# Optimization experiments

Measured on AMD Instinct MI355X. Metric: run time of the kernel, lower is better.

The kernel has to match this reference:

```python
import jax, jax.numpy as jnp
import numpy as np
import math

# dims
B, L, D = 2, 2048, 1024          # batch, seq len, embedding_dim
HID, ATT, H = 1024, 512, 8       # linear_hidden_dim, attention_dim, num_heads
DQK, DUV = ATT // H, HID // H    # 64, 128
NBUCK = 64                       # time_num_buckets
MAX_SPAN = 86400 * 90            # max_time_span
EPS = 1e-6
OUT_DIM = 2 * HID + 2 * ATT      # uvqk output dim = 3072


def _time_boundaries():
    # RelativeAttentionBiasModule._build_boundaries: pure log buckets
    steps = NBUCK - 1
    log_part = np.exp(np.linspace(0.0, math.log(MAX_SPAN), steps))
    b = np.unique(np.floor(np.clip(log_part, 1, None)).astype(np.int64)).astype(np.float32)
    return jnp.asarray(b)

_BOUNDARIES = _time_boundaries()  # len <= 63, indices < NBUCK


def setup_inputs() -> dict:
    key = jax.random.key(0)
    ks = jax.random.split(key, 8)
    x = jax.random.normal(ks[0], (B, L, D), dtype=jnp.float32)
    timestamps = jnp.sort(
        jax.random.randint(ks[1], (B, L), 0, 2592000), axis=-1
    )  # chronological event times (seconds)
    attn_mask = jnp.tril(jnp.ones((L, L), dtype=bool))[None].repeat(B, axis=0)  # causal
    W_uvqk = jax.random.normal(ks[2], (OUT_DIM, D), dtype=jnp.float32) * 0.02
    b_uvqk = jnp.zeros((OUT_DIM,), dtype=jnp.float32)
    time_bias = jax.random.normal(ks[3], (NBUCK, H), dtype=jnp.float32) * 0.02
    W_o = jax.random.normal(ks[4], (D, HID), dtype=jnp.float32) * 0.02
    b_o = jnp.zeros((D,), dtype=jnp.float32)
    rms_w = jnp.ones((HID,), dtype=jnp.float32)
    return {"x": x, "timestamps": timestamps, "attn_mask": attn_mask,
            "W_uvqk": W_uvqk, "b_uvqk": b_uvqk, "time_bias": time_bias,
            "W_o": W_o, "b_o": b_o, "rms_w": rms_w}


def reference(x, timestamps, attn_mask, W_uvqk, b_uvqk, time_bias, W_o, b_o, rms_w):
    Bx, Lx, _ = x.shape
    scale = 1.0 / math.sqrt(DQK)

    # fused uvqk projection + act1 (silu)
    h = jax.nn.silu(x @ W_uvqk.T + b_uvqk)  # [B, L, OUT_DIM]
    u, v, q, k = jnp.split(h, [HID, 2 * HID, 2 * HID + ATT], axis=-1)

    def heads(t, d):  # [B, L, H*d] -> [B, H, L, d]
        return t.reshape(Bx, Lx, H, d).transpose(0, 2, 1, 3)

    u = heads(u, DUV)
    v = heads(v, DUV)
    q = heads(q, DQK) * scale
    k = heads(k, DQK)

    logits = jnp.einsum('bhid,bhjd->bhij', q.astype(jnp.float32), k.astype(jnp.float32))

    # bucketized relative-time bias (per-head)
    tdiff = jnp.abs(timestamps[:, :, None] - timestamps[:, None, :])
    tdiff = jnp.clip(tdiff, 1, None).astype(jnp.float32)  # clamp_min(1)
    bk = jnp.searchsorted(_BOUNDARIES, tdiff, side='left')  # torch.bucketize right=False
    rab = time_bias[bk].transpose(0, 3, 1, 2)  # [B, H, L, L]

    # pointwise silu attention (no softmax), masked
    A = jax.nn.silu(logits + rab) * attn_mask[:, None].astype(jnp.float32)

    y = jnp.einsum('bhij,bhjd->bhid', A, v)               # [B, H, L, DUV]
    y = y.transpose(0, 2, 1, 3).reshape(Bx, Lx, HID)       # merge heads
    u_m = u.transpose(0, 2, 1, 3).reshape(Bx, Lx, HID)

    # RMSNorm then U-gate
    rms = y * jax.lax.rsqrt(jnp.mean(y * y, axis=-1, keepdims=True) + EPS) * rms_w
    y_point = rms.astype(x.dtype) * u_m

    return y_point @ W_o.T + b_o  # [B, L, D]
```

## Files before the change

kernel.cpp:

```cpp
#include <hip/hip_runtime.h>
#include <hip/hip_bf16.h>

typedef float f32x4 __attribute__((ext_vector_type(4)));
typedef short s16x8 __attribute__((ext_vector_type(8)));
typedef short s16x4 __attribute__((ext_vector_type(4)));
typedef unsigned short u16x4 __attribute__((ext_vector_type(4)));

__device__ __forceinline__ float bf2f(unsigned short u) {
    union { unsigned int i; float f; } x; x.i = ((unsigned int)u) << 16; return x.f;
}
__device__ __forceinline__ unsigned short f2bf(float f) {
    union { float f; unsigned int i; } x; x.f = f;
    unsigned int r = x.i + 0x7FFFu + ((x.i >> 16) & 1u);
    return (unsigned short)(r >> 16);
}
__device__ __forceinline__ float silu_fast(float v) {
    return v * __builtin_amdgcn_rcpf(1.f + __expf(-v));
}

#define GLDS16(gp, lp) __builtin_amdgcn_global_load_lds( \
    (const __attribute__((address_space(1))) unsigned int*)(gp), \
    (__attribute__((address_space(3))) unsigned int*)(lp), 16, 0, 0)

__global__ __launch_bounds__(256) void cvt_bucketize(
    const float* __restrict__ X, const float* __restrict__ W,
    const float* __restrict__ Wo, const int* __restrict__ TS,
    unsigned short* __restrict__ Xb, unsigned short* __restrict__ Wb,
    unsigned short* __restrict__ Wob, unsigned char* __restrict__ BK)
{
    const int tid = threadIdx.x;
    if (blockIdx.x < 8192) {
        int idx = blockIdx.x * 256 + tid;
        const float* src; unsigned short* dst; int off;
        if (idx < 1048576)       { src = X;  dst = Xb;  off = idx; }
        else if (idx < 1835008)  { src = W;  dst = Wb;  off = idx - 1048576; }
        else                     { src = Wo; dst = Wob; off = idx - 1835008; }
        f32x4 v = *reinterpret_cast<const f32x4*>(&src[(size_t)off * 4]);
        u16x4 o;
        #pragma unroll
        for (int j = 0; j < 4; ++j) o[j] = f2bf(v[j]);
        *reinterpret_cast<u16x4*>(&dst[(size_t)off * 4]) = o;
        return;
    }
    const int bid = blockIdx.x - 8192;
    const int jt = bid & 31, it = (bid >> 5) & 31, b = bid >> 10;
    if (jt > it) return;
    __shared__ int bndRaw[63];
    __shared__ int bnd[64];
    __shared__ int tsi[64], tsj[64];
    if (tid < 63) {
        double step = log(7776000.0) / 62.0;
        double v = exp(step * (double)tid);
        if (v < 1.0) v = 1.0;
        bndRaw[tid] = (int)floor(v);
    }
    if (tid >= 64 && tid < 128) tsi[tid - 64] = TS[b * 2048 + it * 64 + (tid - 64)];
    else if (tid >= 128 && tid < 192) tsj[tid - 128] = TS[b * 2048 + jt * 64 + (tid - 128)];
    __syncthreads();
    if (tid == 0) {
        int c = 0, p = -1;
        for (int i = 0; i < 63; ++i) { int x = bndRaw[i]; if (x != p) { bnd[c++] = x; p = x; } }
        for (; c < 64; ++c) bnd[c] = 0x7FFFFFFF;
    }
    __syncthreads();
    const int il = tid & 63, jc = (tid >> 6) * 16;
    const int tiv = tsi[il];
    unsigned char out[16];
    #pragma unroll
    for (int u = 0; u < 16; ++u) {
        int td = tiv - tsj[jc + u]; td = td < 0 ? -td : td; if (td < 1) td = 1;
        int pos = 0;
        #pragma unroll
        for (int st = 32; st; st >>= 1)
            if (bnd[pos + st - 1] < td) pos += st;
        out[u] = (unsigned char)pos;
    }
    *reinterpret_cast<int4*>(&BK[((size_t)b << 22) + (size_t)(it * 64 + il) * 2048 + jt * 64 + jc]) =
        *reinterpret_cast<const int4*>(out);
}

__global__ __launch_bounds__(256) void gemm_uvqk(
    const unsigned short* __restrict__ Xb, const unsigned short* __restrict__ Wb,
    const float* __restrict__ bias,
    unsigned short* __restrict__ U, unsigned short* __restrict__ Vt,
    unsigned short* __restrict__ Q, unsigned short* __restrict__ K)
{
    __shared__ __align__(16) unsigned short sA[128][64];
    __shared__ __align__(16) unsigned short sB[128][64];
    const int tid = threadIdx.x;
    const int wv = tid >> 6, lane = tid & 63;
    const int g = lane >> 4, lr = lane & 15;
    const int wid = (blockIdx.x & 7) * 96 + (blockIdx.x >> 3);
    const int m0 = (wid & 31) * 128, n0 = (wid >> 5) * 128;
    const int wr = (wv >> 1) * 64, wc = (wv & 1) * 64;
    const int ls = lr & 7;
    f32x4 acc[4][4] = {};

    for (int k0 = 0; k0 < 1024; k0 += 64) {
        #pragma unroll
        for (int c = 0; c < 4; ++c) {
            int id = c * 256 + tid;
            int row = id >> 3, c8 = id & 7;
            int sc = (c8 ^ (row & 7)) * 8;
            GLDS16(&Xb[(size_t)(m0 + row) * 1024 + k0 + sc], &sA[row][c8 * 8]);
            GLDS16(&Wb[(size_t)(n0 + row) * 1024 + k0 + sc], &sB[row][c8 * 8]);
        }
        __syncthreads();
        #pragma unroll
        for (int kq = 0; kq < 2; ++kq) {
            s16x8 afr[4], bfr[4];
            #pragma unroll
            for (int i = 0; i < 4; ++i) {
                afr[i] = *reinterpret_cast<const s16x8*>(
                    &sA[wr + i * 16 + lr][((kq * 4 + g) ^ ls) * 8]);
                bfr[i] = *reinterpret_cast<const s16x8*>(
                    &sB[wc + i * 16 + lr][((kq * 4 + g) ^ ls) * 8]);
            }
            #pragma unroll
            for (int mi = 0; mi < 4; ++mi)
                #pragma unroll
                for (int ni = 0; ni < 4; ++ni)
                    acc[mi][ni] = __builtin_amdgcn_mfma_f32_16x16x32_bf16(
                        afr[mi], bfr[ni], acc[mi][ni], 0, 0, 0);
        }
        __syncthreads();
    }

    if (n0 >= 1024 && n0 < 2048) {
        const int head = (n0 - 1024) >> 7;
        unsigned short* sT = &sA[0][0] + wv * (32 * 72);
        #pragma unroll
        for (int hh = 0; hh < 2; ++hh) {
            #pragma unroll
            for (int nn = 0; nn < 2; ++nn) {
                int ni = hh * 2 + nn;
                float bn = bias[n0 + wc + ni * 16 + lr];
                #pragma unroll
                for (int mi = 0; mi < 4; ++mi)
                    #pragma unroll
                    for (int r = 0; r < 4; ++r)
                        sT[(nn * 16 + lr) * 72 + mi * 16 + g * 4 + r] =
                            f2bf(silu_fast(acc[mi][ni][r] + bn));
            }
            #pragma unroll
            for (int c = 0; c < 4; ++c) {
                int id = c * 64 + lane;
                int row = id >> 3, ch = id & 7;
                s16x8 val = *reinterpret_cast<const s16x8*>(&sT[row * 72 + ch * 8]);
                int d = wc + hh * 32 + row;
                int mg = m0 + wr + ch * 8;
                int bb = mg >> 11, l = mg & 2047;
                *reinterpret_cast<s16x8*>(
                    &Vt[(((size_t)(bb * 8 + head) * 128 + d) << 11) + l]) = val;
            }
        }
    } else {
        #pragma unroll
        for (int ni = 0; ni < 4; ++ni) {
            int n = n0 + wc + ni * 16 + lr;
            float bn = bias[n];
            #pragma unroll
            for (int mi = 0; mi < 4; ++mi) {
                #pragma unroll
                for (int r = 0; r < 4; ++r) {
                    int m = m0 + wr + mi * 16 + g * 4 + r;
                    float v = silu_fast(acc[mi][ni][r] + bn);
                    int b = m >> 11, l = m & 2047;
                    if (n < 1024) {
                        U[(size_t)m * 1024 + n] = f2bf(v);
                    } else if (n < 2560) {
                        int dd = n - 2048, h = dd >> 6, d = dd & 63;
                        Q[((((size_t)(b * 8 + h) << 11) + l) << 6) + d] = f2bf(v * 0.125f);
                    } else {
                        int dd = n - 2560, h = dd >> 6, d = dd & 63;
                        K[((((size_t)(b * 8 + h) << 11) + l) << 6) + d] = f2bf(v);
                    }
                }
            }
        }
    }
}

__global__ __launch_bounds__(512, 4) void attn(
    const unsigned short* __restrict__ Q, const unsigned short* __restrict__ K,
    const unsigned short* __restrict__ Vt, const unsigned char* __restrict__ BK,
    const float* __restrict__ TB, unsigned short* __restrict__ Y)
{
    __shared__ __align__(16) char smem[49152];

    const int tid = threadIdx.x, wv = tid >> 6, lane = tid & 63;
    const int g = lane >> 4, lr = lane & 15;

    const int bid = blockIdx.x;
    const int xcd = bid & 7, kix = bid >> 3;
    const int bh = 2 * xcd + (kix & 1);
    const int ti = 31 - (kix >> 1);
    const int b = bh >> 3, h = bh & 7;
    const int i0 = ti * 64;
    const int rg = wv & 3;
    const int half = wv >> 2;
    const int irow = i0 + rg * 16;
    const int P = ti + 1;

    const int tbl = __float_as_int(TB[lane * 8 + h]);

    const unsigned short* qb = Q + ((size_t)bh << 11) * 64;
    const unsigned short* kb = K + ((size_t)bh << 11) * 64;
    const unsigned short* vtb = Vt + ((size_t)bh << 7) * 2048;
    const unsigned char* bkp = BK + ((size_t)b << 22) + (size_t)(irow + lr) * 2048 + g * 4;

    s16x8 aq[2];
    #pragma unroll
    for (int kq = 0; kq < 2; ++kq)
        aq[kq] = *reinterpret_cast<const s16x8*>(&qb[(size_t)(irow + lr) * 64 + kq * 32 + g * 8]);

    char* base = smem;
    const int cs = lr & 7;
    const int ib = irow + lr;

    auto stage = [&](int p, int db) {
        const int j0e = p * 64;
        char* kd = base + db * 8192;
        char* vd = base + 16384 + db * 16384;
        {
            int r = tid >> 3, c8 = tid & 7;
            int jr = r & 31, hk = r >> 5;
            GLDS16(kb + (size_t)(j0e + hk * 32 + jr) * 64 + ((c8 ^ (jr & 7)) * 8),
                   kd + tid * 16);
        }
        #pragma unroll
        for (int c = 0; c < 2; ++c) {
            int id = c * 512 + tid;
            int d = id >> 3, L = id & 7;
            int hv = L >> 2, c16 = L & 3;
            GLDS16(vtb + (size_t)d * 2048 + j0e + hv * 32 + ((c16 ^ (d & 3)) * 8),
                   vd + id * 16);
        }
    };

#define BIAS_LOAD(p, bw) { const unsigned char* p_ = bkp + (size_t)(2 * (p) + half) * 32; \
        bw[0] = *(const unsigned int*)(p_); bw[1] = *(const unsigned int*)(p_ + 16); }

    f32x4 accy[8] = {};

#define COMPUTE(DB, BW, p) { \
        const int jt = 2 * (p) + half; \
        const char* kbase = base + (DB) * 8192 + half * 4096; \
        f32x4 sacc[2] = {}; \
        _Pragma("unroll") \
        for (int ni = 0; ni < 2; ++ni) { \
            _Pragma("unroll") \
            for (int kq = 0; kq < 2; ++kq) { \
                s16x8 kf = *reinterpret_cast<const s16x8*>( \
                    kbase + (ni * 16 + lr) * 128 + (((kq * 4 + g) ^ cs) << 4)); \
                sacc[ni] = __builtin_amdgcn_mfma_f32_16x16x32_bf16(kf, aq[kq], sacc[ni], 0, 0, 0); \
            } \
        } \
        const int j0 = jt * 32; \
        const bool diag = ((p) == P - 1); \
        s16x4 pf[2]; \
        _Pragma("unroll") \
        for (int ni = 0; ni < 2; ++ni) { \
            unsigned int bw = BW[ni]; \
            float b0 = __int_as_float(__builtin_amdgcn_ds_bpermute((int)((bw & 255u) << 2), tbl)); \
            float b1 = __int_as_float(__builtin_amdgcn_ds_bpermute((int)(((bw >> 8) & 255u) << 2), tbl)); \
            float b2 = __int_as_float(__builtin_amdgcn_ds_bpermute((int)(((bw >> 16) & 255u) << 2), tbl)); \
            float b3 = __int_as_float(__builtin_amdgcn_ds_bpermute((int)((bw >> 24) << 2), tbl)); \
            float v0 = silu_fast(sacc[ni][0] + b0); \
            float v1 = silu_fast(sacc[ni][1] + b1); \
            float v2 = silu_fast(sacc[ni][2] + b2); \
            float v3 = silu_fast(sacc[ni][3] + b3); \
            if (diag) { \
                int jb = j0 + ni * 16 + g * 4; \
                if (jb + 0 > ib) v0 = 0.f; \
                if (jb + 1 > ib) v1 = 0.f; \
                if (jb + 2 > ib) v2 = 0.f; \
                if (jb + 3 > ib) v3 = 0.f; \
            } \
            unsigned int w0, w1; \
            asm("v_cvt_pk_bf16_f32 %0, %1, %2" : "=v"(w0) : "v"(v0), "v"(v1)); \
            asm("v_cvt_pk_bf16_f32 %0, %1, %2" : "=v"(w1) : "v"(v2), "v"(v3)); \
            union { unsigned int u_[2]; s16x4 v_; } cvt_; \
            cvt_.u_[0] = w0; cvt_.u_[1] = w1; \
            pf[ni] = cvt_.v_; \
        } \
        const char* vbase = base + 16384 + (DB) * 16384 + half * 64; \
        _Pragma("unroll") \
        for (int di = 0; di < 8; ++di) { \
            _Pragma("unroll") \
            for (int ni = 0; ni < 2; ++ni) { \
                s16x4 vf = *reinterpret_cast<const s16x4*>( \
                    vbase + (di * 16 + lr) * 128 + ((((ni << 1) + (g >> 1)) ^ (lr & 3)) << 4) + ((g & 1) << 3)); \
                accy[di] = __builtin_amdgcn_mfma_f32_16x16x16bf16_1k(pf[ni], vf, accy[di], 0, 0, 0); \
            } \
        } }

    unsigned int bwA[2], bwB[2];
    stage(0, 0);
    BIAS_LOAD(0, bwA);

    int p = 0;
    for (;;) {
        __builtin_amdgcn_s_barrier();
        if (p + 1 < P) {
            stage(p + 1, 1);
            BIAS_LOAD(p + 1, bwB);
            asm volatile("s_waitcnt vmcnt(5)" ::: "memory");
        } else {
            asm volatile("s_waitcnt vmcnt(0)" ::: "memory");
        }
        __builtin_amdgcn_s_barrier();
        COMPUTE(0, bwA, p);
        if (++p == P) break;
        __builtin_amdgcn_s_barrier();
        if (p + 1 < P) {
            stage(p + 1, 0);
            BIAS_LOAD(p + 1, bwA);
            asm volatile("s_waitcnt vmcnt(5)" ::: "memory");
        } else {
            asm volatile("s_waitcnt vmcnt(0)" ::: "memory");
        }
        __builtin_amdgcn_s_barrier();
        COMPUTE(1, bwB, p);
        if (++p == P) break;
    }
#undef COMPUTE
#undef BIAS_LOAD

    __syncthreads();
    float* red = (float*)base;
    if (wv >= 4) {
        #pragma unroll
        for (int di = 0; di < 8; ++di)
            #pragma unroll
            for (int r = 0; r < 4; ++r)
                red[(rg * 16 + g * 4 + r) * 132 + di * 16 + lr] = accy[di][r];
    }
    __syncthreads();
    if (wv < 4) {
        #pragma unroll
        for (int di = 0; di < 8; ++di)
            #pragma unroll
            for (int r = 0; r < 4; ++r) {
                float s = accy[di][r] + red[(rg * 16 + g * 4 + r) * 132 + di * 16 + lr];
                Y[(size_t)((b << 11) + irow + g * 4 + r) * 1024 + h * 128 + di * 16 + lr] = f2bf(s);
            }
    }
}

__global__ __launch_bounds__(256) void rmsnorm_gate(
    const unsigned short* __restrict__ Y, const unsigned short* __restrict__ U,
    const float* __restrict__ rw, unsigned short* __restrict__ YP)
{
    __shared__ float red[4];
    const int row = blockIdx.x, tid = threadIdx.x;
    u16x4 v4 = *reinterpret_cast<const u16x4*>(&Y[(size_t)row * 1024 + tid * 4]);
    float v[4];
    #pragma unroll
    for (int j = 0; j < 4; ++j) v[j] = bf2f(v4[j]);
    float ss = v[0] * v[0] + v[1] * v[1] + v[2] * v[2] + v[3] * v[3];
    #pragma unroll
    for (int off = 32; off; off >>= 1) ss += __shfl_down(ss, off);
    if ((tid & 63) == 0) red[tid >> 6] = ss;
    __syncthreads();
    float rms = rsqrtf((red[0] + red[1] + red[2] + red[3]) * (1.f / 1024.f) + 1e-6f);
    #pragma unroll
    for (int j = 0; j < 4; ++j) {
        int c = tid * 4 + j;
        float o = v[j] * rms * rw[c] * bf2f(U[(size_t)row * 1024 + c]);
        YP[(size_t)row * 1024 + c] = f2bf(o);
    }
}

__global__ __launch_bounds__(512) void gemm_out(
    const unsigned short* __restrict__ YP, const unsigned short* __restrict__ Wob,
    const float* __restrict__ bo, float* __restrict__ OUT)
{
    __shared__ __align__(16) unsigned short sA[128][64];
    __shared__ __align__(16) unsigned short sB[128][64];
    const int tid = threadIdx.x;
    const int wv = tid >> 6, lane = tid & 63;
    const int g = lane >> 4, lr = lane & 15;
    const int wid = (blockIdx.x & 7) * 32 + (blockIdx.x >> 3);
    const int m0 = (wid & 31) * 128, n0 = (wid >> 5) * 128;
    const int wr = (wv >> 2) * 64, wc = (wv & 3) * 32;
    const int ls = lr & 7;
    f32x4 acc[4][2] = {};

    for (int k0 = 0; k0 < 1024; k0 += 64) {
        #pragma unroll
        for (int c = 0; c < 2; ++c) {
            int id = c * 512 + tid;
            int row = id >> 3, c8 = id & 7;
            int sc = (c8 ^ (row & 7)) * 8;
            GLDS16(&YP[(size_t)(m0 + row) * 1024 + k0 + sc], &sA[row][c8 * 8]);
            GLDS16(&Wob[(size_t)(n0 + row) * 1024 + k0 + sc], &sB[row][c8 * 8]);
        }
        __syncthreads();
        #pragma unroll
        for (int kq = 0; kq < 2; ++kq) {
            s16x8 afr[4], bfr[2];
            #pragma unroll
            for (int i = 0; i < 4; ++i)
                afr[i] = *reinterpret_cast<const s16x8*>(
                    &sA[wr + i * 16 + lr][((kq * 4 + g) ^ ls) * 8]);
            #pragma unroll
            for (int i = 0; i < 2; ++i)
                bfr[i] = *reinterpret_cast<const s16x8*>(
                    &sB[wc + i * 16 + lr][((kq * 4 + g) ^ ls) * 8]);
            #pragma unroll
            for (int mi = 0; mi < 4; ++mi)
                #pragma unroll
                for (int ni = 0; ni < 2; ++ni)
                    acc[mi][ni] = __builtin_amdgcn_mfma_f32_16x16x32_bf16(
                        afr[mi], bfr[ni], acc[mi][ni], 0, 0, 0);
        }
        __syncthreads();
    }

    #pragma unroll
    for (int ni = 0; ni < 2; ++ni) {
        int n = n0 + wc + ni * 16 + lr;
        float bn = bo[n];
        #pragma unroll
        for (int mi = 0; mi < 4; ++mi)
            #pragma unroll
            for (int r = 0; r < 4; ++r) {
                int m = m0 + wr + mi * 16 + g * 4 + r;
                OUT[(size_t)m * 1024 + n] = acc[mi][ni][r] + bn;
            }
    }
}

extern "C" void kernel_launch(void* const* d_in, const int* in_sizes, int n_in,
                              void* d_out, int out_size, void* d_ws, size_t ws_size,
                              hipStream_t stream) {
    const float* X     = (const float*)d_in[0];
    const int*   TS    = (const int*)d_in[1];
    const float* Wuvqk = (const float*)d_in[3];
    const float* buvqk = (const float*)d_in[4];
    const float* TB    = (const float*)d_in[5];
    const float* Wo    = (const float*)d_in[6];
    const float* bo    = (const float*)d_in[7];
    const float* rw    = (const float*)d_in[8];
    float* OUT = (float*)d_out;

    char* ws = (char*)d_ws;
    unsigned short* Qb  = (unsigned short*)(ws);
    unsigned short* Kb  = (unsigned short*)(ws + (4u << 20));
    unsigned short* Vt  = (unsigned short*)(ws + (8u << 20));
    unsigned short* Ub  = (unsigned short*)(ws + (16u << 20));
    unsigned short* Yb  = (unsigned short*)(ws + (24u << 20));
    unsigned short* Xb  = (unsigned short*)(ws + (24u << 20));
    unsigned short* Wb  = (unsigned short*)(ws + (32u << 20));
    unsigned short* YP  = (unsigned short*)(ws + (40u << 20));
    unsigned char*  BKm = (unsigned char*)(ws + (48u << 20));
    unsigned short* Wob = (unsigned short*)(ws + (56u << 20));

    cvt_bucketize<<<10240, 256, 0, stream>>>(X, Wuvqk, Wo, TS, Xb, Wb, Wob, BKm);
    gemm_uvqk<<<768, 256, 0, stream>>>(Xb, Wb, buvqk, Ub, Vt, Qb, Kb);
    attn<<<512, 512, 0, stream>>>(Qb, Kb, Vt, BKm, TB, Yb);
    rmsnorm_gate<<<4096, 256, 0, stream>>>(Yb, Ub, rw, YP);
    gemm_out<<<256, 512, 0, stream>>>(YP, Wob, bo, OUT);
}
```

Baseline: 166.9 us.

## Split attention KV range across two blocks with partial outputs summed in rmsnorm

Restructures the attention work split. Each block now owns 128 query rows (one 16-row strip per wave) and half of the causal KV range, taking either the first or the second half of the tiles. Partial outputs go to two bf16 buffers that rmsnorm_gate adds. This removes the intra-block LDS reduction between wave halves and evens out per-block work across the causal triangle. Waves whose diagonal is passed skip compute. The cost is extra Y traffic, bf16 rounding of the partials before summing, and a reshuffled workspace layout that aliases Yb0/Yb1 onto the Xb/Wb regions.

```diff
diff --git a/kernel.cpp b/kernel.cpp
--- a/kernel.cpp
+++ b/kernel.cpp
@@ -184,7 +184,8 @@
 __global__ __launch_bounds__(512, 4) void attn(
     const unsigned short* __restrict__ Q, const unsigned short* __restrict__ K,
     const unsigned short* __restrict__ Vt, const unsigned char* __restrict__ BK,
-    const float* __restrict__ TB, unsigned short* __restrict__ Y)
+    const float* __restrict__ TB,
+    unsigned short* __restrict__ Yb0, unsigned short* __restrict__ Yb1)
 {
     __shared__ __align__(16) char smem[49152];
 
@@ -192,15 +193,17 @@
     const int g = lane >> 4, lr = lane & 15;
 
     const int bid = blockIdx.x;
-    const int xcd = bid & 7, kix = bid >> 3;
-    const int bh = 2 * xcd + (kix & 1);
-    const int ti = 31 - (kix >> 1);
+    const int xcd = bid & 7, r_ = bid >> 3;
+    const int bh = 2 * xcd + (r_ & 1);
+    const int k2 = r_ >> 1;
+    const int st = 15 - (k2 >> 1);
+    const int jh = k2 & 1;
     const int b = bh >> 3, h = bh & 7;
-    const int i0 = ti * 64;
-    const int rg = wv & 3;
-    const int half = wv >> 2;
-    const int irow = i0 + rg * 16;
-    const int P = ti + 1;
+    const int i0 = st << 7;
+    const int irow = i0 + wv * 16;
+    const int jt0 = jh ? (st + 1) : 0;
+    const int P = st + 1;
+    const int diagT = irow >> 6;
 
     const int tbl = __float_as_int(TB[lane * 8 + h]);
 
@@ -208,6 +211,7 @@
     const unsigned short* kb = K + ((size_t)bh << 11) * 64;
     const unsigned short* vtb = Vt + ((size_t)bh << 7) * 2048;
     const unsigned char* bkp = BK + ((size_t)b << 22) + (size_t)(irow + lr) * 2048 + g * 4;
+    unsigned short* Yp = jh ? Yb1 : Yb0;
 
     s16x8 aq[2];
     #pragma unroll
@@ -218,146 +222,134 @@
     const int cs = lr & 7;
     const int ib = irow + lr;
 
-    auto stage = [&](int p, int db) {
-        const int j0e = p * 64;
+    auto stage = [&](int jt, int db) {
+        const size_t j0 = (size_t)jt * 64;
         char* kd = base + db * 8192;
         char* vd = base + 16384 + db * 16384;
         {
-            int r = tid >> 3, c8 = tid & 7;
-            int jr = r & 31, hk = r >> 5;
-            GLDS16(kb + (size_t)(j0e + hk * 32 + jr) * 64 + ((c8 ^ (jr & 7)) * 8),
-                   kd + tid * 16);
+            int row = tid >> 3, c8 = tid & 7;
+            GLDS16(kb + (j0 + row) * 64 + ((c8 ^ (row & 7)) * 8), kd + tid * 16);
         }
         #pragma unroll
         for (int c = 0; c < 2; ++c) {
             int id = c * 512 + tid;
-            int d = id >> 3, L = id & 7;
-            int hv = L >> 2, c16 = L & 3;
-            GLDS16(vtb + (size_t)d * 2048 + j0e + hv * 32 + ((c16 ^ (d & 3)) * 8),
-                   vd + id * 16);
+            int d = id >> 3, c8 = id & 7;
+            GLDS16(vtb + (size_t)d * 2048 + j0 + ((c8 ^ (d & 7)) * 8), vd + id * 16);
         }
     };
 
-#define BIAS_LOAD(p, bw) { const unsigned char* p_ = bkp + (size_t)(2 * (p) + half) * 32; \
-        bw[0] = *(const unsigned int*)(p_); bw[1] = *(const unsigned int*)(p_ + 16); }
+#define BIAS_LOAD(jt, bw) { const unsigned char* p_ = bkp + (size_t)(jt) * 64; \
+        bw[0] = *(const unsigned int*)(p_);      bw[1] = *(const unsigned int*)(p_ + 16); \
+        bw[2] = *(const unsigned int*)(p_ + 32); bw[3] = *(const unsigned int*)(p_ + 48); }
 
     f32x4 accy[8] = {};
 
-#define COMPUTE(DB, BW, p) { \
-        const int jt = 2 * (p) + half; \
-        const char* kbase = base + (DB) * 8192 + half * 4096; \
-        f32x4 sacc[2] = {}; \
-        _Pragma("unroll") \
-        for (int ni = 0; ni < 2; ++ni) { \
+#define COMPUTE(DB, BW, jt) { \
+        if ((jt) <= diagT) { \
+            const char* kbase = base + (DB) * 8192; \
+            f32x4 sacc[4] = {}; \
             _Pragma("unroll") \
-            for (int kq = 0; kq < 2; ++kq) { \
-                s16x8 kf = *reinterpret_cast<const s16x8*>( \
-                    kbase + (ni * 16 + lr) * 128 + (((kq * 4 + g) ^ cs) << 4)); \
-                sacc[ni] = __builtin_amdgcn_mfma_f32_16x16x32_bf16(kf, aq[kq], sacc[ni], 0, 0, 0); \
+            for (int ni = 0; ni < 4; ++ni) { \
+                _Pragma("unroll") \
+                for (int kq = 0; kq < 2; ++kq) { \
+                    s16x8 kf = *reinterpret_cast<const s16x8*>( \
+                        kbase + (ni * 16 + lr) * 128 + (((kq * 4 + g) ^ cs) << 4)); \
+                    sacc[ni] = __builtin_amdgcn_mfma_f32_16x16x32_bf16(kf, aq[kq], sacc[ni], 0, 0, 0); \
+                } \
             } \
-        } \
-        const int j0 = jt * 32; \
-        const bool diag = ((p) == P - 1); \
-        s16x4 pf[2]; \
-        _Pragma("unroll") \
-        for (int ni = 0; ni < 2; ++ni) { \
-            unsigned int bw = BW[ni]; \
-            float b0 = __int_as_float(__builtin_amdgcn_ds_bpermute((int)((bw & 255u) << 2), tbl)); \
-            float b1 = __int_as_float(__builtin_amdgcn_ds_bpermute((int)(((bw >> 8) & 255u) << 2), tbl)); \
-            float b2 = __int_as_float(__builtin_amdgcn_ds_bpermute((int)(((bw >> 16) & 255u) << 2), tbl)); \
-            float b3 = __int_as_float(__builtin_amdgcn_ds_bpermute((int)((bw >> 24) << 2), tbl)); \
-            float v0 = silu_fast(sacc[ni][0] + b0); \
-            float v1 = silu_fast(sacc[ni][1] + b1); \
-            float v2 = silu_fast(sacc[ni][2] + b2); \
-            float v3 = silu_fast(sacc[ni][3] + b3); \
-            if (diag) { \
-                int jb = j0 + ni * 16 + g * 4; \
-                if (jb + 0 > ib) v0 = 0.f; \
-                if (jb + 1 > ib) v1 = 0.f; \
-                if (jb + 2 > ib) v2 = 0.f; \
-                if (jb + 3 > ib) v3 = 0.f; \
+            const int j0 = (jt) * 64; \
+            const bool diag = ((jt) == diagT); \
+            s16x4 pf[4]; \
+            _Pragma("unroll") \
+            for (int ni = 0; ni < 4; ++ni) { \
+                unsigned int bw = BW[ni]; \
+                float b0 = __int_as_float(__builtin_amdgcn_ds_bpermute((int)((bw & 255u) << 2), tbl)); \
+                float b1 = __int_as_float(__builtin_amdgcn_ds_bpermute((int)(((bw >> 8) & 255u) << 2), tbl)); \
+                float b2 = __int_as_float(__builtin_amdgcn_ds_bpermute((int)(((bw >> 16) & 255u) << 2), tbl)); \
+                float b3 = __int_as_float(__builtin_amdgcn_ds_bpermute((int)((bw >> 24) << 2), tbl)); \
+                float v0 = silu_fast(sacc[ni][0] + b0); \
+                float v1 = silu_fast(sacc[ni][1] + b1); \
+                float v2 = silu_fast(sacc[ni][2] + b2); \
+                float v3 = silu_fast(sacc[ni][3] + b3); \
+                if (diag) { \
+                    int jb = j0 + ni * 16 + g * 4; \
+                    if (jb + 0 > ib) v0 = 0.f; \
+                    if (jb + 1 > ib) v1 = 0.f; \
+                    if (jb + 2 > ib) v2 = 0.f; \
+                    if (jb + 3 > ib) v3 = 0.f; \
+                } \
+                unsigned int w0, w1; \
+                asm("v_cvt_pk_bf16_f32 %0, %1, %2" : "=v"(w0) : "v"(v0), "v"(v1)); \
+                asm("v_cvt_pk_bf16_f32 %0, %1, %2" : "=v"(w1) : "v"(v2), "v"(v3)); \
+                union { unsigned int u_[2]; s16x4 v_; } cvt_; \
+                cvt_.u_[0] = w0; cvt_.u_[1] = w1; \
+                pf[ni] = cvt_.v_; \
             } \
-            unsigned int w0, w1; \
-            asm("v_cvt_pk_bf16_f32 %0, %1, %2" : "=v"(w0) : "v"(v0), "v"(v1)); \
-            asm("v_cvt_pk_bf16_f32 %0, %1, %2" : "=v"(w1) : "v"(v2), "v"(v3)); \
-            union { unsigned int u_[2]; s16x4 v_; } cvt_; \
-            cvt_.u_[0] = w0; cvt_.u_[1] = w1; \
-            pf[ni] = cvt_.v_; \
-        } \
-        const char* vbase = base + 16384 + (DB) * 16384 + half * 64; \
-        _Pragma("unroll") \
-        for (int di = 0; di < 8; ++di) { \
+            const char* vbase = base + 16384 + (DB) * 16384; \
             _Pragma("unroll") \
-            for (int ni = 0; ni < 2; ++ni) { \
-                s16x4 vf = *reinterpret_cast<const s16x4*>( \
-                    vbase + (di * 16 + lr) * 128 + ((((ni << 1) + (g >> 1)) ^ (lr & 3)) << 4) + ((g & 1) << 3)); \
-                accy[di] = __builtin_amdgcn_mfma_f32_16x16x16bf16_1k(pf[ni], vf, accy[di], 0, 0, 0); \
+            for (int di = 0; di < 8; ++di) { \
+                _Pragma("unroll") \
+                for (int ni = 0; ni < 4; ++ni) { \
+                    s16x4 vf = *reinterpret_cast<const s16x4*>( \
+                        vbase + (di * 16 + lr) * 128 + (((2 * ni + (g >> 1)) ^ cs) << 4) + ((g & 1) << 3)); \
+                    accy[di] = __builtin_amdgcn_mfma_f32_16x16x16bf16_1k(pf[ni], vf, accy[di], 0, 0, 0); \
+                } \
             } \
         } }
 
-    unsigned int bwA[2], bwB[2];
-    stage(0, 0);
-    BIAS_LOAD(0, bwA);
+    unsigned int bwA[4], bwB[4];
+    stage(jt0, 0);
+    BIAS_LOAD(jt0, bwA);
 
     int p = 0;
     for (;;) {
         __builtin_amdgcn_s_barrier();
         if (p + 1 < P) {
-            stage(p + 1, 1);
-            BIAS_LOAD(p + 1, bwB);
-            asm volatile("s_waitcnt vmcnt(5)" ::: "memory");
+            stage(jt0 + p + 1, 1);
+            BIAS_LOAD(jt0 + p + 1, bwB);
+            asm volatile("s_waitcnt vmcnt(7)" ::: "memory");
         } else {
             asm volatile("s_waitcnt vmcnt(0)" ::: "memory");
         }
         __builtin_amdgcn_s_barrier();
-        COMPUTE(0, bwA, p);
+        COMPUTE(0, bwA, jt0 + p);
         if (++p == P) break;
         __builtin_amdgcn_s_barrier();
         if (p + 1 < P) {
-            stage(p + 1, 0);
-            BIAS_LOAD(p + 1, bwA);
-            asm volatile("s_waitcnt vmcnt(5)" ::: "memory");
+            stage(jt0 + p + 1, 0);
+            BIAS_LOAD(jt0 + p + 1, bwA);
+            asm volatile("s_waitcnt vmcnt(7)" ::: "memory");
         } else {
             asm volatile("s_waitcnt vmcnt(0)" ::: "memory");
         }
         __builtin_amdgcn_s_barrier();
-        COMPUTE(1, bwB, p);
+        COMPUTE(1, bwB, jt0 + p);
         if (++p == P) break;
     }
 #undef COMPUTE
 #undef BIAS_LOAD
 
-    __syncthreads();
-    float* red = (float*)base;
-    if (wv >= 4) {
-        #pragma unroll
-        for (int di = 0; di < 8; ++di)
-            #pragma unroll
-            for (int r = 0; r < 4; ++r)
-                red[(rg * 16 + g * 4 + r) * 132 + di * 16 + lr] = accy[di][r];
-    }
-    __syncthreads();
-    if (wv < 4) {
-        #pragma unroll
-        for (int di = 0; di < 8; ++di)
-            #pragma unroll
-            for (int r = 0; r < 4; ++r) {
-                float s = accy[di][r] + red[(rg * 16 + g * 4 + r) * 132 + di * 16 + lr];
-                Y[(size_t)((b << 11) + irow + g * 4 + r) * 1024 + h * 128 + di * 16 + lr] = f2bf(s);
-            }
-    }
+    #pragma unroll
+    for (int di = 0; di < 8; ++di)
+        #pragma unroll
+        for (int r = 0; r < 4; ++r) {
+            int i = irow + g * 4 + r;
+            Yp[(size_t)((b << 11) + i) * 1024 + h * 128 + di * 16 + lr] = f2bf(accy[di][r]);
+        }
 }
 
 __global__ __launch_bounds__(256) void rmsnorm_gate(
-    const unsigned short* __restrict__ Y, const unsigned short* __restrict__ U,
+    const unsigned short* __restrict__ Y0, const unsigned short* __restrict__ Y1,
+    const unsigned short* __restrict__ U,
     const float* __restrict__ rw, unsigned short* __restrict__ YP)
 {
     __shared__ float red[4];
     const int row = blockIdx.x, tid = threadIdx.x;
-    u16x4 v4 = *reinterpret_cast<const u16x4*>(&Y[(size_t)row * 1024 + tid * 4]);
+    u16x4 a4 = *reinterpret_cast<const u16x4*>(&Y0[(size_t)row * 1024 + tid * 4]);
+    u16x4 b4 = *reinterpret_cast<const u16x4*>(&Y1[(size_t)row * 1024 + tid * 4]);
     float v[4];
     #pragma unroll
-    for (int j = 0; j < 4; ++j) v[j] = bf2f(v4[j]);
+    for (int j = 0; j < 4; ++j) v[j] = bf2f(a4[j]) + bf2f(b4[j]);
     float ss = v[0] * v[0] + v[1] * v[1] + v[2] * v[2] + v[3] * v[3];
     #pragma unroll
     for (int off = 32; off; off >>= 1) ss += __shfl_down(ss, off);
@@ -450,16 +442,17 @@
     unsigned short* Kb  = (unsigned short*)(ws + (4u << 20));
     unsigned short* Vt  = (unsigned short*)(ws + (8u << 20));
     unsigned short* Ub  = (unsigned short*)(ws + (16u << 20));
-    unsigned short* Yb  = (unsigned short*)(ws + (24u << 20));
-    unsigned short* Xb  = (unsigned short*)(ws + (24u << 20));
-    unsigned short* Wb  = (unsigned short*)(ws + (32u << 20));
-    unsigned short* YP  = (unsigned short*)(ws + (40u << 20));
-    unsigned char*  BKm = (unsigned char*)(ws + (48u << 20));
-    unsigned short* Wob = (unsigned short*)(ws + (56u << 20));
+    unsigned char*  BKm = (unsigned char*)(ws + (24u << 20));
+    unsigned short* Xb  = (unsigned short*)(ws + (32u << 20));
+    unsigned short* Wb  = (unsigned short*)(ws + (40u << 20));
+    unsigned short* Yb0 = (unsigned short*)(ws + (32u << 20));
+    unsigned short* Yb1 = (unsigned short*)(ws + (40u << 20));
+    unsigned short* Wob = (unsigned short*)(ws + (48u << 20));
+    unsigned short* YP  = (unsigned short*)(ws + (50u << 20));
 
     cvt_bucketize<<<10240, 256, 0, stream>>>(X, Wuvqk, Wo, TS, Xb, Wb, Wob, BKm);
     gemm_uvqk<<<768, 256, 0, stream>>>(Xb, Wb, buvqk, Ub, Vt, Qb, Kb);
-    attn<<<512, 512, 0, stream>>>(Qb, Kb, Vt, BKm, TB, Yb);
-    rmsnorm_gate<<<4096, 256, 0, stream>>>(Yb, Ub, rw, YP);
+    attn<<<512, 512, 0, stream>>>(Qb, Kb, Vt, BKm, TB, Yb0, Yb1);
+    rmsnorm_gate<<<4096, 256, 0, stream>>>(Yb0, Yb1, Ub, rw, YP);
     gemm_out<<<256, 512, 0, stream>>>(YP, Wob, bo, OUT);
 }
```

Result: faster. 147.1 us (-11.9%).
